# Kernel tuning notes

Hardware: AMD Instinct MI355X
Metric: run time of the kernel (lower is better)

The kernel has to match this reference:

```python
import jax, jax.numpy as jnp
import numpy as np

B, C, H, W, N = 32, 256, 56, 56, 1024


def setup_inputs() -> dict:
    key = jax.random.key(0)
    k1, k2, k3, k4 = jax.random.split(key, 4)
    x = jax.random.normal(k1, (B, C, H, W), dtype=jnp.float32)
    W_s = jax.random.normal(k2, (N, H, W), dtype=jnp.float32)
    W_d = jax.random.normal(k3, (N, C, 1, 1), dtype=jnp.float32)
    W_b = jax.random.normal(k4, (1, N), dtype=jnp.float32)
    return {"x": x, "W_s": W_s, "W_d": W_d, "W_b": W_b}


def reference(x, W_s, W_d, W_b):
    # Original: out = einsum('bchw,nhw->bnchw'); per-neuron 1x1 conv with W_d[n]
    # (C -> 1 channel); sum over (c,h,w); add bias. Mathematically:
    #   out[b,n] = sum_{c,h,w} x[b,c,h,w] * W_s[n,h,w] * W_d[n,c] + W_b[0,n]
    # Computed without materializing the (B,N,C,H,W) blow-up:
    y = jnp.einsum('bchw,nhw->bnc', x, W_s)          # spatial contraction
    out = jnp.einsum('bnc,nc->bn', y, W_d[:, :, 0, 0])  # channel contraction
    return out + W_b
```

## Files before the change

kernel.cpp:

```cpp
#include <hip/hip_runtime.h>
#include <stdint.h>


#define K_DIM 3136
#define N_DIM 1024
#define C_DIM 256
#define B_DIM 32
#define M_DIM 8192
#define WS_ELEMS (N_DIM * K_DIM)

typedef __attribute__((ext_vector_type(8))) short short8v;
typedef __attribute__((ext_vector_type(4))) float f32x4;
typedef __attribute__((ext_vector_type(4))) unsigned int uint4v;

__device__ __forceinline__ short f2bf(float f) {
  union { float f; unsigned u; } v; v.f = f;
  unsigned r = v.u + 0x7FFFu + ((v.u >> 16) & 1u);
  return (short)(r >> 16);
}

__device__ __forceinline__ unsigned pk2bf(float a, float b) {
  unsigned ua = __float_as_uint(a) + 0x8000u;
  unsigned ub = __float_as_uint(b) + 0x8000u;
  return (ua >> 16) | (ub & 0xFFFF0000u);
}

__device__ __forceinline__ void async16(const void* g, void* l) {
  __builtin_amdgcn_global_load_lds(
      (const __attribute__((address_space(1))) unsigned int*)g,
      (__attribute__((address_space(3))) unsigned int*)l, 16, 0, 0);
}

#define WSBLK (WS_ELEMS / 2048)
__global__ __launch_bounds__(256) void convert_ws_bias(
    const float* __restrict__ Ws, const float* __restrict__ Wb,
    short* __restrict__ dst, float* __restrict__ out) {
  int bid = blockIdx.x;
  if (bid >= WSBLK) {
    int i = (bid - WSBLK) * 256 + threadIdx.x;
    out[i] = Wb[i & (N_DIM - 1)];
    return;
  }
  size_t i = (size_t)bid * 2048 + threadIdx.x * 8;
  f32x4 v0 = __builtin_nontemporal_load((const f32x4*)(Ws + i));
  f32x4 v1 = __builtin_nontemporal_load((const f32x4*)(Ws + i) + 1);
  short8v s;
  s[0] = f2bf(v0.x); s[1] = f2bf(v0.y); s[2] = f2bf(v0.z); s[3] = f2bf(v0.w);
  s[4] = f2bf(v1.x); s[5] = f2bf(v1.y); s[6] = f2bf(v1.z); s[7] = f2bf(v1.w);
  *(short8v*)(dst + i) = s;
}

__global__ __launch_bounds__(512, 4) void gemm_fused(
    const float* __restrict__ x, const short* __restrict__ Bbf,
    const float* __restrict__ Wd, float* __restrict__ out) {
  __shared__ __align__(16) short As[256 * 64];
  __shared__ __align__(16) short Bs[128 * 64];

  const int bid = blockIdx.x;
  const int mt = bid & 31;
  const int nt = (bid >> 5) & 7;
  const int z = bid >> 8;
  const int kt0 = z * 25;
  const int ktn = z ? 24 : 25;

  const int t = threadIdx.x;
  const int lane = t & 63;
  const int wv = t >> 6;
  const int r = lane & 15;
  const int q = lane >> 4;
  const int wm = wv >> 1, wn = wv & 1;

  const int rr = lane >> 3;
  const int k8 = (lane & 7) ^ rr;
  const short* Bw = Bbf + (size_t)(nt * 128 + wv * 16 + rr) * K_DIM + k8 * 8 + kt0 * 64;
  char* BsB = (char*)Bs + wv * 2048;

  const int rr8 = lane >> 3;
  const int c8 = lane & 7;
  const int slotA = c8 ^ rr8;
  const float* Aw =
      x + (size_t)(mt * 256 + wv * 32 + rr8) * K_DIM + kt0 * 64 + c8 * 8;
  short* AsW = As + (wv * 32 + rr8) * 64 + slotA * 8;

  f32x4 acc[4][4];
#pragma unroll
  for (int i = 0; i < 4; ++i)
#pragma unroll
    for (int j = 0; j < 4; ++j) acc[i][j] = (f32x4)0.0f;

  for (int kt = 0; kt < ktn; ++kt) {
    __syncthreads();
#pragma unroll
    for (int p = 0; p < 2; ++p)
      async16(Bw + (size_t)p * 8 * K_DIM + kt * 64, BsB + p * 1024);
#pragma unroll
    for (int w = 0; w < 4; ++w) {
      const float* g = Aw + (size_t)w * 8 * K_DIM + kt * 64;
      f32x4 va = *(const f32x4*)g;
      f32x4 vb = *(const f32x4*)(g + 4);
      uint4v u;
      u.x = pk2bf(va.x, va.y);
      u.y = pk2bf(va.z, va.w);
      u.z = pk2bf(vb.x, vb.y);
      u.w = pk2bf(vb.z, vb.w);
      *(uint4v*)(AsW + (size_t)w * 8 * 64) = u;
    }
    __syncthreads();

#pragma unroll
    for (int ks = 0; ks < 2; ++ks) {
      const int xo = ((ks * 4 + q) ^ (r & 7)) * 16;
      short8v a[4], b[4];
#pragma unroll
      for (int i = 0; i < 4; ++i)
        a[i] = *(const short8v*)((const char*)As + (64 * wm + 16 * i + r) * 128 + xo);
#pragma unroll
      for (int j = 0; j < 4; ++j)
        b[j] = *(const short8v*)((const char*)Bs + (64 * wn + 16 * j + r) * 128 + xo);
#pragma unroll
      for (int i = 0; i < 4; ++i)
#pragma unroll
        for (int j = 0; j < 4; ++j)
          acc[i][j] = __builtin_amdgcn_mfma_f32_16x16x32_bf16(a[i], b[j],
                                                              acc[i][j], 0, 0, 0);
    }
  }

#pragma unroll
  for (int j = 0; j < 4; ++j) {
    const int n_g = nt * 128 + 64 * wn + 16 * j + r;
    float p = 0.0f;
#pragma unroll
    for (int i = 0; i < 4; ++i) {
      const int c_l = 64 * wm + 16 * i + 4 * q;
      const float4 wd = *(const float4*)(Wd + (size_t)n_g * C_DIM + c_l);
      p += acc[i][j].x * wd.x + acc[i][j].y * wd.y + acc[i][j].z * wd.z +
           acc[i][j].w * wd.w;
    }
    p += __shfl_xor(p, 16, 64);
    p += __shfl_xor(p, 32, 64);
    if (q == 0) atomicAdd(&out[(size_t)mt * N_DIM + n_g], p);
  }
}

extern "C" void kernel_launch(void* const* d_in, const int* in_sizes, int n_in,
                              void* d_out, int out_size, void* d_ws, size_t ws_size,
                              hipStream_t stream) {
  const float* x = (const float*)d_in[0];
  const float* Ws = (const float*)d_in[1];
  const float* Wd = (const float*)d_in[2];
  const float* Wb = (const float*)d_in[3];
  float* out = (float*)d_out;
  short* wsbf = (short*)d_ws;

  convert_ws_bias<<<dim3(WSBLK + 128), dim3(256), 0, stream>>>(Ws, Wb, wsbf, out);
  gemm_fused<<<dim3(32 * 8 * 2), dim3(512), 0, stream>>>(x, wsbf, Wd, out);
}
```

Before: 237.1 us.

## Load x tiles as fp32 via async global-to-LDS and convert at fragment read

The A operand (x) is now copied from global memory straight into LDS as fp32 with async global_load_lds, using an XOR swizzle, instead of going through registers, being converted to bf16 and stored to LDS. The bf16 conversion moves to after the LDS fragment read in the MFMA loop. This removes the register round-trip and the VALU work from the load path, so loads can be asynchronous. In exchange the A tile in LDS doubles in size (64KB for A plus 16KB for B), which cuts occupancy, and conversion work is added in the inner loop.

```diff
diff --git a/kernel.cpp b/kernel.cpp
--- a/kernel.cpp
+++ b/kernel.cpp
@@ -53,7 +53,7 @@
 __global__ __launch_bounds__(512, 4) void gemm_fused(
     const float* __restrict__ x, const short* __restrict__ Bbf,
     const float* __restrict__ Wd, float* __restrict__ out) {
-  __shared__ __align__(16) short As[256 * 64];
+  __shared__ __align__(16) float As[256 * 64];
   __shared__ __align__(16) short Bs[128 * 64];
 
   const int bid = blockIdx.x;
@@ -70,17 +70,21 @@
   const int q = lane >> 4;
   const int wm = wv >> 1, wn = wv & 1;
 
-  const int rr = lane >> 3;
-  const int k8 = (lane & 7) ^ rr;
-  const short* Bw = Bbf + (size_t)(nt * 128 + wv * 16 + rr) * K_DIM + k8 * 8 + kt0 * 64;
+  const int rr8 = lane >> 3;
+  const int k8 = (lane & 7) ^ rr8;
+  const short* Bw = Bbf + (size_t)(nt * 128 + wv * 16 + rr8) * K_DIM + k8 * 8 + kt0 * 64;
   char* BsB = (char*)Bs + wv * 2048;
 
-  const int rr8 = lane >> 3;
-  const int c8 = lane & 7;
-  const int slotA = c8 ^ rr8;
-  const float* Aw =
-      x + (size_t)(mt * 256 + wv * 32 + rr8) * K_DIM + kt0 * 64 + c8 * 8;
-  short* AsW = As + (wv * 32 + rr8) * 64 + slotA * 8;
+  const int rr4 = lane >> 4;
+  const int s16 = lane & 15;
+  const float* Ap[8];
+#pragma unroll
+  for (int p = 0; p < 8; ++p) {
+    const int row = wv * 32 + p * 4 + rr4;
+    const int g = s16 ^ (row & 15);
+    Ap[p] = x + (size_t)(mt * 256 + row) * K_DIM + kt0 * 64 + g * 4;
+  }
+  char* AsW = (char*)As + wv * 8192;
 
   f32x4 acc[4][4];
 #pragma unroll
@@ -91,38 +95,36 @@
   for (int kt = 0; kt < ktn; ++kt) {
     __syncthreads();
 #pragma unroll
+    for (int p = 0; p < 8; ++p)
+      async16(Ap[p] + kt * 64, AsW + p * 1024);
+#pragma unroll
     for (int p = 0; p < 2; ++p)
       async16(Bw + (size_t)p * 8 * K_DIM + kt * 64, BsB + p * 1024);
-#pragma unroll
-    for (int w = 0; w < 4; ++w) {
-      const float* g = Aw + (size_t)w * 8 * K_DIM + kt * 64;
-      f32x4 va = *(const f32x4*)g;
-      f32x4 vb = *(const f32x4*)(g + 4);
-      uint4v u;
-      u.x = pk2bf(va.x, va.y);
-      u.y = pk2bf(va.z, va.w);
-      u.z = pk2bf(vb.x, vb.y);
-      u.w = pk2bf(vb.z, vb.w);
-      *(uint4v*)(AsW + (size_t)w * 8 * 64) = u;
-    }
     __syncthreads();
 
 #pragma unroll
     for (int ks = 0; ks < 2; ++ks) {
+      const int h2 = 8 * ks + 2 * q;
       const int xo = ((ks * 4 + q) ^ (r & 7)) * 16;
-      short8v a[4], b[4];
-#pragma unroll
-      for (int i = 0; i < 4; ++i)
-        a[i] = *(const short8v*)((const char*)As + (64 * wm + 16 * i + r) * 128 + xo);
+      short8v b[4];
 #pragma unroll
       for (int j = 0; j < 4; ++j)
         b[j] = *(const short8v*)((const char*)Bs + (64 * wn + 16 * j + r) * 128 + xo);
 #pragma unroll
-      for (int i = 0; i < 4; ++i)
+      for (int i = 0; i < 4; ++i) {
+        const char* rowp = (const char*)As + (64 * wm + 16 * i + r) * 256;
+        f32x4 va = *(const f32x4*)(rowp + ((h2 ^ r) * 16));
+        f32x4 vb = *(const f32x4*)(rowp + (((h2 + 1) ^ r) * 16));
+        union { uint4v u; short8v s; } cvt;
+        cvt.u.x = pk2bf(va.x, va.y);
+        cvt.u.y = pk2bf(va.z, va.w);
+        cvt.u.z = pk2bf(vb.x, vb.y);
+        cvt.u.w = pk2bf(vb.z, vb.w);
 #pragma unroll
         for (int j = 0; j < 4; ++j)
-          acc[i][j] = __builtin_amdgcn_mfma_f32_16x16x32_bf16(a[i], b[j],
+          acc[i][j] = __builtin_amdgcn_mfma_f32_16x16x32_bf16(cvt.s, b[j],
                                                               acc[i][j], 0, 0, 0);
+      }
     }
   }
 
```

After: 232.6 us. Within noise of the previous version (-1.9%).
